# Performance work log

Measured on AMD Instinct MI355X. Metric: run time of the kernel, lower is better.

Reference implementation:

```python
import jax, jax.numpy as jnp
import numpy as np

EMBED = 1024  # point_net_embedding_dim
H1, H2 = 512, 256  # head_hidden_layer_sizes


def _init(key, shape, fan_in):
    return jax.random.normal(key, shape, dtype=jnp.float32) / jnp.sqrt(jnp.float32(fan_in))


def setup_inputs() -> dict:
    key = jax.random.key(0)
    ks = jax.random.split(key, 13)
    B, N = 256, 1024
    x = jax.random.normal(ks[0], (B, N, 3), dtype=jnp.float32)
    # PointNet shared per-point MLP: 3 -> 64 -> 128 -> EMBED (ReLU), max-pool over points
    W1 = _init(ks[1], (3, 64), 3);        b1 = jnp.zeros((64,), jnp.float32)
    W2 = _init(ks[2], (64, 128), 64);     b2 = jnp.zeros((128,), jnp.float32)
    W3 = _init(ks[3], (128, EMBED), 128); b3 = jnp.zeros((EMBED,), jnp.float32)
    # Head MLP: EMBED -> 512 -> 256 -> 9 (no final activation)
    Wh1 = _init(ks[4], (EMBED, H1), EMBED); bh1 = jnp.zeros((H1,), jnp.float32)
    Wh2 = _init(ks[5], (H1, H2), H1);       bh2 = jnp.zeros((H2,), jnp.float32)
    Wh3 = _init(ks[6], (H2, 9), H2);        bh3 = jnp.zeros((9,), jnp.float32)
    return {"x": x, "W1": W1, "b1": b1, "W2": W2, "b2": b2, "W3": W3, "b3": b3,
            "Wh1": Wh1, "bh1": bh1, "Wh2": Wh2, "bh2": bh2, "Wh3": Wh3, "bh3": bh3}


def svd_projection(M):
    # Project raw 3x3 matrices onto SO(3): R = U diag(1,1,det(U V^T)) V^T
    U, S, Vh = jnp.linalg.svd(M, full_matrices=False)
    det = jnp.linalg.det(jnp.einsum('...ij,...jk->...ik', U, Vh))
    d = jnp.stack([jnp.ones_like(det), jnp.ones_like(det), det], axis=-1)  # [..., 3]
    return jnp.einsum('...ij,...j,...jk->...ik', U, d, Vh)


def reference(x, W1, b1, W2, b2, W3, b3, Wh1, bh1, Wh2, bh2, Wh3, bh3):
    # Shared per-point MLP (ReLU), final_activation=ReLU, then max-pool over points
    h = jax.nn.relu(x @ W1 + b1)          # [B, N, 64]
    h = jax.nn.relu(h @ W2 + b2)          # [B, N, 128]
    h = jax.nn.relu(h @ W3 + b3)          # [B, N, EMBED]
    g = jnp.max(h, axis=-2)               # [B, EMBED] global feature
    # Head MLP -> raw 3x3
    z = jax.nn.relu(g @ Wh1 + bh1)
    z = jax.nn.relu(z @ Wh2 + bh2)
    raw = (z @ Wh3 + bh3).reshape(*x.shape[:-2], 3, 3)
    return svd_projection(raw)
```

## Files before the change

kernel.cpp:

```cpp
#include <hip/hip_runtime.h>
#include <math.h>

typedef _Float16 f16;
typedef _Float16 f16x8 __attribute__((ext_vector_type(8)));
typedef float f32x4 __attribute__((ext_vector_type(4)));

__global__ __launch_bounds__(256) void prep_weights(
    const float* __restrict__ W1, const float* __restrict__ b1,
    const float* __restrict__ W2, const float* __restrict__ W3,
    f16* __restrict__ W2t, f16* __restrict__ W3t, float* __restrict__ wpk)
{
    int idx = blockIdx.x * 256 + threadIdx.x;
    int stride = gridDim.x * 256;
    for (int i = idx; i < 1024 * 128; i += stride) {
        int c = i >> 7, k = i & 127;
        W3t[i] = (f16)W3[k * 1024 + c];
    }
    for (int i = idx; i < 128 * 64; i += stride) {
        int c = i >> 6, k = i & 63;
        W2t[i] = (f16)W2[k * 128 + c];
    }
    if (idx < 256) {
        int k = idx >> 2, c = idx & 3;
        wpk[idx] = (c < 3) ? W1[c * 64 + k] : b1[k];
    }
}

__global__ __launch_bounds__(512, 2) void pointnet_fused(
    const float* __restrict__ x,
    const float* __restrict__ wpk,
    const f16* __restrict__ W2t,
    const float* __restrict__ b2,
    const f16* __restrict__ W3t,
    const float* __restrict__ b3,
    float* __restrict__ g)
{
    __shared__ float xs[1024 * 3];
    __shared__ __align__(16) float wls[288];
    __shared__ float b2s[128];
    __shared__ __align__(16) f16 h2s[2][128 * 136];

    int b = blockIdx.x;
    int tid = threadIdx.x;
    int lane = tid & 63, w = tid >> 6;
    int lrow = lane & 15, quad = lane >> 4;
    int wr2 = w & 3, wc2 = w >> 2;

    f16x8 bf3[8][4];
    {
        const f16* base = W3t + (size_t)(w * 128 + lrow) * 128 + quad * 8;
#pragma unroll
        for (int ct = 0; ct < 8; ct++)
#pragma unroll
            for (int kc = 0; kc < 4; kc++)
                bf3[ct][kc] = *(const f16x8*)(base + ct * 16 * 128 + kc * 32);
    }
    f16x8 bf2[4][2];
    {
        const f16* base = W2t + (size_t)(wc2 * 64 + lrow) * 64 + quad * 8;
#pragma unroll
        for (int ct = 0; ct < 4; ct++)
#pragma unroll
            for (int kc2 = 0; kc2 < 2; kc2++)
                bf2[ct][kc2] = *(const f16x8*)(base + ct * 16 * 64 + kc2 * 32);
    }

    {
        const float* xb = x + (size_t)b * 3072;
        for (int i = tid; i < 3072; i += 512) xs[i] = xb[i];
        if (tid < 256) {
            int k = tid >> 2, c = tid & 3;
            wls[(k + (k >> 3)) * 4 + c] = wpk[tid];
        }
        if (tid >= 256 && tid < 384) b2s[tid - 256] = b2[tid - 256];
    }
    __syncthreads();

    const f32x4 z4 = {0.f, 0.f, 0.f, 0.f};
    float cmax[8];
#pragma unroll
    for (int ct = 0; ct < 8; ct++) cmax[ct] = -3.0e38f;

    auto phaseA = [&](int chunk) {
        f16* hb = h2s[chunk & 1];
        int p0 = chunk * 128 + wr2 * 32 + lrow;
        float x00 = xs[p0 * 3], x01 = xs[p0 * 3 + 1], x02 = xs[p0 * 3 + 2];
        int p1 = p0 + 16;
        float x10 = xs[p1 * 3], x11 = xs[p1 * 3 + 1], x12 = xs[p1 * 3 + 2];
        f32x4 acc2[2][4];
#pragma unroll
        for (int kc2 = 0; kc2 < 2; kc2++) {
            f16x8 af2[2];
#pragma unroll
            for (int j = 0; j < 8; j++) {
                int k = kc2 * 32 + quad * 8 + j;
                f32x4 wv = *(const f32x4*)&wls[(k + (k >> 3)) * 4];
                float v0 = fmaf(x02, wv[2], fmaf(x01, wv[1], fmaf(x00, wv[0], wv[3])));
                float v1 = fmaf(x12, wv[2], fmaf(x11, wv[1], fmaf(x10, wv[0], wv[3])));
                af2[0][j] = (f16)fmaxf(v0, 0.f);
                af2[1][j] = (f16)fmaxf(v1, 0.f);
            }
#pragma unroll
            for (int rt = 0; rt < 2; rt++)
#pragma unroll
                for (int ct = 0; ct < 4; ct++)
                    acc2[rt][ct] = __builtin_amdgcn_mfma_f32_16x16x32_f16(
                        af2[rt], bf2[ct][kc2], kc2 ? acc2[rt][ct] : z4, 0, 0, 0);
        }
#pragma unroll
        for (int rt = 0; rt < 2; rt++)
#pragma unroll
            for (int ct = 0; ct < 4; ct++) {
                int col = wc2 * 64 + ct * 16 + lrow;
                float bb = b2s[col];
                int rowb = wr2 * 32 + rt * 16 + quad * 4;
#pragma unroll
                for (int r = 0; r < 4; r++)
                    hb[(rowb + r) * 136 + col] = (f16)fmaxf(acc2[rt][ct][r] + bb, 0.f);
            }
    };

    auto phaseB = [&](int chunk) {
        const f16* hb = h2s[chunk & 1];
#pragma unroll
        for (int rt = 0; rt < 8; rt++) {
            f32x4 acc[8];
#pragma unroll
            for (int kc = 0; kc < 4; kc++) {
                f16x8 af = *(const f16x8*)(hb + (rt * 16 + lrow) * 136 + kc * 32 + quad * 8);
#pragma unroll
                for (int ct = 0; ct < 8; ct++)
                    acc[ct] = __builtin_amdgcn_mfma_f32_16x16x32_f16(
                        af, bf3[ct][kc], kc ? acc[ct] : z4, 0, 0, 0);
            }
#pragma unroll
            for (int ct = 0; ct < 8; ct++) {
                float m01 = fmaxf(acc[ct][0], acc[ct][1]);
                float m23 = fmaxf(acc[ct][2], acc[ct][3]);
                cmax[ct] = fmaxf(cmax[ct], fmaxf(m01, m23));
            }
        }
    };

    phaseA(0);
    __syncthreads();
#pragma unroll 1
    for (int c = 0; c < 7; c++) {
        phaseA(c + 1);
        phaseB(c);
        __syncthreads();
    }
    phaseB(7);

#pragma unroll
    for (int ct = 0; ct < 8; ct++) {
        cmax[ct] = fmaxf(cmax[ct], __shfl_xor(cmax[ct], 16, 64));
        cmax[ct] = fmaxf(cmax[ct], __shfl_xor(cmax[ct], 32, 64));
    }
    if (quad == 0) {
#pragma unroll
        for (int ct = 0; ct < 8; ct++) {
            int cg = w * 128 + ct * 16 + lrow;
            g[(size_t)b * 1024 + cg] = fmaxf(cmax[ct] + b3[cg], 0.f);
        }
    }
}

__global__ __launch_bounds__(256) void head_l1(
    const float* __restrict__ g, const float* __restrict__ Wh1,
    float* __restrict__ zp1)
{
    __shared__ float gs4[4][256];
    int cb = blockIdx.x, bb = blockIdx.y, kc = blockIdx.z;
    int tid = threadIdx.x;
    int b0 = bb * 4;
    int kbase = kc * 256;
#pragma unroll
    for (int j = 0; j < 4; j++) {
        int i = tid + j * 256;
        gs4[i >> 8][i & 255] = g[(size_t)(b0 + (i >> 8)) * 1024 + kbase + (i & 255)];
    }
    __syncthreads();

    int c = cb * 256 + tid;
    float acc[4] = {0.f, 0.f, 0.f, 0.f};
#pragma unroll 1
    for (int k = 0; k < 256; k += 8) {
        float w[8];
#pragma unroll
        for (int j = 0; j < 8; j++) w[j] = Wh1[(size_t)(kbase + k + j) * 512 + c];
#pragma unroll
        for (int r = 0; r < 4; r++) {
            float4 a = *(const float4*)&gs4[r][k];
            float4 bq = *(const float4*)&gs4[r][k + 4];
            acc[r] = fmaf(a.x, w[0], acc[r]);
            acc[r] = fmaf(a.y, w[1], acc[r]);
            acc[r] = fmaf(a.z, w[2], acc[r]);
            acc[r] = fmaf(a.w, w[3], acc[r]);
            acc[r] = fmaf(bq.x, w[4], acc[r]);
            acc[r] = fmaf(bq.y, w[5], acc[r]);
            acc[r] = fmaf(bq.z, w[6], acc[r]);
            acc[r] = fmaf(bq.w, w[7], acc[r]);
        }
    }
#pragma unroll
    for (int r = 0; r < 4; r++)
        zp1[((size_t)kc * 256 + b0 + r) * 512 + c] = acc[r];
}

__global__ __launch_bounds__(256) void head_l2(
    const float* __restrict__ zp1, const float* __restrict__ bh1,
    const float* __restrict__ Wh2, float* __restrict__ zp2)
{
    __shared__ float z1s[2][128];
    int bb = blockIdx.x, kc2 = blockIdx.y;
    int tid = threadIdx.x;
    int b0 = bb * 2;
    int kb = kc2 * 128;
    {
        int row = tid >> 7, kk = tid & 127;
        int col = kb + kk;
        float v = bh1[col];
#pragma unroll
        for (int j = 0; j < 4; j++)
            v += zp1[((size_t)j * 256 + b0 + row) * 512 + col];
        z1s[row][kk] = fmaxf(v, 0.f);
    }
    __syncthreads();

    int c = tid;
    float acc0 = 0.f, acc1 = 0.f;
#pragma unroll 1
    for (int k = 0; k < 128; k += 8) {
        float w[8];
#pragma unroll
        for (int j = 0; j < 8; j++) w[j] = Wh2[(size_t)(kb + k + j) * 256 + c];
        float4 a0 = *(const float4*)&z1s[0][k];
        float4 a1 = *(const float4*)&z1s[0][k + 4];
        float4 d0 = *(const float4*)&z1s[1][k];
        float4 d1 = *(const float4*)&z1s[1][k + 4];
        acc0 = fmaf(a0.x, w[0], acc0);  acc1 = fmaf(d0.x, w[0], acc1);
        acc0 = fmaf(a0.y, w[1], acc0);  acc1 = fmaf(d0.y, w[1], acc1);
        acc0 = fmaf(a0.z, w[2], acc0);  acc1 = fmaf(d0.z, w[2], acc1);
        acc0 = fmaf(a0.w, w[3], acc0);  acc1 = fmaf(d0.w, w[3], acc1);
        acc0 = fmaf(a1.x, w[4], acc0);  acc1 = fmaf(d1.x, w[4], acc1);
        acc0 = fmaf(a1.y, w[5], acc0);  acc1 = fmaf(d1.y, w[5], acc1);
        acc0 = fmaf(a1.z, w[6], acc0);  acc1 = fmaf(d1.z, w[6], acc1);
        acc0 = fmaf(a1.w, w[7], acc0);  acc1 = fmaf(d1.w, w[7], acc1);
    }
    zp2[((size_t)kc2 * 256 + b0    ) * 256 + c] = acc0;
    zp2[((size_t)kc2 * 256 + b0 + 1) * 256 + c] = acc1;
}

__device__ inline void jrot(double S[3][3], double V[3][3], int p, int q)
{
    double apq = S[p][q];
    if (fabs(apq) < 1e-36) return;
    double tau = (S[q][q] - S[p][p]) / (2.0 * apq);
    double t = (tau >= 0.0 ? 1.0 : -1.0) / (fabs(tau) + sqrt(1.0 + tau * tau));
    double c = 1.0 / sqrt(1.0 + t * t);
    double s = t * c;
    for (int k = 0; k < 3; k++) {
        double skp = S[k][p], skq = S[k][q];
        S[k][p] = c * skp - s * skq;  S[k][q] = s * skp + c * skq;
    }
    for (int k = 0; k < 3; k++) {
        double spk = S[p][k], sqk = S[q][k];
        S[p][k] = c * spk - s * sqk;  S[q][k] = s * spk + c * sqk;
    }
    for (int k = 0; k < 3; k++) {
        double vkp = V[k][p], vkq = V[k][q];
        V[k][p] = c * vkp - s * vkq;  V[k][q] = s * vkp + c * vkq;
    }
}

__device__ void svd_so3(const float* Mf, float* Rout)
{
    double M[3][3], S[3][3], V[3][3];
    for (int i = 0; i < 3; i++)
        for (int j = 0; j < 3; j++) M[i][j] = (double)Mf[3 * i + j];
    for (int i = 0; i < 3; i++)
        for (int j = 0; j < 3; j++)
            S[i][j] = M[0][i] * M[0][j] + M[1][i] * M[1][j] + M[2][i] * M[2][j];
    for (int i = 0; i < 3; i++)
        for (int j = 0; j < 3; j++) V[i][j] = (i == j) ? 1.0 : 0.0;
    for (int it = 0; it < 10; it++) {
        jrot(S, V, 0, 1); jrot(S, V, 0, 2); jrot(S, V, 1, 2);
    }
    double lam[3] = {S[0][0], S[1][1], S[2][2]};
    int i0 = 0, i1 = 1, i2 = 2, tt;
    if (lam[i0] < lam[i1]) { tt = i0; i0 = i1; i1 = tt; }
    if (lam[i0] < lam[i2]) { tt = i0; i0 = i2; i2 = tt; }
    if (lam[i1] < lam[i2]) { tt = i1; i1 = i2; i2 = tt; }
    double v0[3], v1[3], v2[3];
    for (int k = 0; k < 3; k++) { v0[k] = V[k][i0]; v1[k] = V[k][i1]; v2[k] = V[k][i2]; }
    double u1[3], u2[3], u3[3];
    for (int i = 0; i < 3; i++) u1[i] = M[i][0] * v0[0] + M[i][1] * v0[1] + M[i][2] * v0[2];
    double n1 = sqrt(u1[0] * u1[0] + u1[1] * u1[1] + u1[2] * u1[2]) + 1e-300;
    for (int i = 0; i < 3; i++) u1[i] /= n1;
    for (int i = 0; i < 3; i++) u2[i] = M[i][0] * v1[0] + M[i][1] * v1[1] + M[i][2] * v1[2];
    double d12 = u1[0] * u2[0] + u1[1] * u2[1] + u1[2] * u2[2];
    for (int i = 0; i < 3; i++) u2[i] -= d12 * u1[i];
    double n2 = sqrt(u2[0] * u2[0] + u2[1] * u2[1] + u2[2] * u2[2]) + 1e-300;
    for (int i = 0; i < 3; i++) u2[i] /= n2;
    u3[0] = u1[1] * u2[2] - u1[2] * u2[1];
    u3[1] = u1[2] * u2[0] - u1[0] * u2[2];
    u3[2] = u1[0] * u2[1] - u1[1] * u2[0];
    double c12x = v1[1] * v2[2] - v1[2] * v2[1];
    double c12y = v1[2] * v2[0] - v1[0] * v2[2];
    double c12z = v1[0] * v2[1] - v1[1] * v2[0];
    double detV = v0[0] * c12x + v0[1] * c12y + v0[2] * c12z;
    for (int i = 0; i < 3; i++)
        for (int j = 0; j < 3; j++)
            Rout[3 * i + j] = (float)(u1[i] * v0[j] + u2[i] * v1[j] + detV * u3[i] * v2[j]);
}

__global__ __launch_bounds__(128) void head_l3_svd(
    const float* __restrict__ zp2, const float* __restrict__ bh2,
    const float* __restrict__ Wh3, const float* __restrict__ bh3,
    float* __restrict__ out)
{
    __shared__ float z2s[8][256];
    __shared__ float wh3s[2304];
    __shared__ float raws[8][12];
    int b0 = blockIdx.x * 8;
    int tid = threadIdx.x;

    for (int i = tid; i < 2304; i += 128) wh3s[i] = Wh3[i];
    for (int i = tid; i < 8 * 256; i += 128) {
        int row = i >> 8, kk = i & 255;
        float v = bh2[kk];
#pragma unroll
        for (int j = 0; j < 4; j++)
            v += zp2[((size_t)j * 256 + b0 + row) * 256 + kk];
        z2s[row][kk] = fmaxf(v, 0.f);
    }
    __syncthreads();

    if (tid < 72) {
        int r = tid / 9, c = tid % 9;
        float acc = bh3[c];
#pragma unroll 8
        for (int k = 0; k < 256; k++) acc = fmaf(z2s[r][k], wh3s[k * 9 + c], acc);
        raws[r][c] = acc;
    }
    __syncthreads();

    if (tid < 8) svd_so3(&raws[tid][0], out + (size_t)(b0 + tid) * 9);
}

extern "C" void kernel_launch(void* const* d_in, const int* in_sizes, int n_in,
                              void* d_out, int out_size, void* d_ws, size_t ws_size,
                              hipStream_t stream)
{
    const float* x   = (const float*)d_in[0];
    const float* W1  = (const float*)d_in[1];
    const float* b1  = (const float*)d_in[2];
    const float* W2  = (const float*)d_in[3];
    const float* b2  = (const float*)d_in[4];
    const float* W3  = (const float*)d_in[5];
    const float* b3  = (const float*)d_in[6];
    const float* Wh1 = (const float*)d_in[7];
    const float* bh1 = (const float*)d_in[8];
    const float* Wh2 = (const float*)d_in[9];
    const float* bh2 = (const float*)d_in[10];
    const float* Wh3 = (const float*)d_in[11];
    const float* bh3 = (const float*)d_in[12];
    float* out = (float*)d_out;

    char* ws = (char*)d_ws;
    f16*   W2t = (f16*)ws;
    f16*   W3t = (f16*)(ws + 65536);
    float* wpk = (float*)(ws + 524288);
    float* g   = (float*)(ws + 1048576);
    float* zp1 = (float*)(ws + 2097152);
    float* zp2 = (float*)(ws + 4194304);

    prep_weights<<<128, 256, 0, stream>>>(W1, b1, W2, W3, W2t, W3t, wpk);
    pointnet_fused<<<256, 512, 0, stream>>>(x, wpk, W2t, b2, W3t, b3, g);
    dim3 gridH1(2, 64, 4);
    head_l1<<<gridH1, 256, 0, stream>>>(g, Wh1, zp1);
    dim3 gridH2(128, 4);
    head_l2<<<gridH2, 256, 0, stream>>>(zp1, bh1, Wh2, zp2);
    head_l3_svd<<<32, 128, 0, stream>>>(zp2, bh2, Wh3, bh3, out);
}
```

Measured before the change: 177.6 us.

## Split point max-pool across two blocks per cloud and fuse head MLP kernels

The per-point MLP kernel now launches two blocks per batch element, each handling 512 points and writing a partial max. The head applies the final max, bias and ReLU, then runs all three head layers and the SVD projection in one kernel. This removes two intermediate launches and the split-K partial buffers, and doubles the block count to fill more CUs. It also raises the launch-bounds occupancy hint and pads the LDS row stride to 140, which adds register pressure and spill risk given the large per-thread W3 fragment array; each head block now streams the full Wh1 and Wh2.

```diff
diff --git a/kernel.cpp b/kernel.cpp
--- a/kernel.cpp
+++ b/kernel.cpp
@@ -4,6 +4,8 @@
 typedef _Float16 f16;
 typedef _Float16 f16x8 __attribute__((ext_vector_type(8)));
 typedef float f32x4 __attribute__((ext_vector_type(4)));
+
+#define H2_STRIDE 140
 
 __global__ __launch_bounds__(256) void prep_weights(
     const float* __restrict__ W1, const float* __restrict__ b1,
@@ -26,21 +28,21 @@
     }
 }
 
-__global__ __launch_bounds__(512, 2) void pointnet_fused(
+__global__ __launch_bounds__(512, 4) void pointnet_fused(
     const float* __restrict__ x,
     const float* __restrict__ wpk,
     const f16* __restrict__ W2t,
     const float* __restrict__ b2,
     const f16* __restrict__ W3t,
-    const float* __restrict__ b3,
-    float* __restrict__ g)
-{
-    __shared__ float xs[1024 * 3];
+    float* __restrict__ gpart)
+{
+    __shared__ float xs[512 * 3];
     __shared__ __align__(16) float wls[288];
     __shared__ float b2s[128];
-    __shared__ __align__(16) f16 h2s[2][128 * 136];
-
-    int b = blockIdx.x;
+    __shared__ __align__(16) f16 h2s[2][128 * H2_STRIDE];
+
+    int bid = blockIdx.x;
+    int b = bid & 255, half = bid >> 8;
     int tid = threadIdx.x;
     int lane = tid & 63, w = tid >> 6;
     int lrow = lane & 15, quad = lane >> 4;
@@ -66,8 +68,8 @@
     }
 
     {
-        const float* xb = x + (size_t)b * 3072;
-        for (int i = tid; i < 3072; i += 512) xs[i] = xb[i];
+        const float* xb = x + (size_t)b * 3072 + (size_t)half * 1536;
+        for (int i = tid; i < 1536; i += 512) xs[i] = xb[i];
         if (tid < 256) {
             int k = tid >> 2, c = tid & 3;
             wls[(k + (k >> 3)) * 4 + c] = wpk[tid];
@@ -116,7 +118,7 @@
                 int rowb = wr2 * 32 + rt * 16 + quad * 4;
 #pragma unroll
                 for (int r = 0; r < 4; r++)
-                    hb[(rowb + r) * 136 + col] = (f16)fmaxf(acc2[rt][ct][r] + bb, 0.f);
+                    hb[(rowb + r) * H2_STRIDE + col] = (f16)fmaxf(acc2[rt][ct][r] + bb, 0.f);
             }
     };
 
@@ -127,7 +129,7 @@
             f32x4 acc[8];
 #pragma unroll
             for (int kc = 0; kc < 4; kc++) {
-                f16x8 af = *(const f16x8*)(hb + (rt * 16 + lrow) * 136 + kc * 32 + quad * 8);
+                f16x8 af = *(const f16x8*)(hb + (rt * 16 + lrow) * H2_STRIDE + kc * 32 + quad * 8);
 #pragma unroll
                 for (int ct = 0; ct < 8; ct++)
                     acc[ct] = __builtin_amdgcn_mfma_f32_16x16x32_f16(
@@ -145,12 +147,12 @@
     phaseA(0);
     __syncthreads();
 #pragma unroll 1
-    for (int c = 0; c < 7; c++) {
+    for (int c = 0; c < 3; c++) {
         phaseA(c + 1);
         phaseB(c);
         __syncthreads();
     }
-    phaseB(7);
+    phaseB(3);
 
 #pragma unroll
     for (int ct = 0; ct < 8; ct++) {
@@ -161,95 +163,91 @@
 #pragma unroll
         for (int ct = 0; ct < 8; ct++) {
             int cg = w * 128 + ct * 16 + lrow;
-            g[(size_t)b * 1024 + cg] = fmaxf(cmax[ct] + b3[cg], 0.f);
-        }
-    }
-}
-
-__global__ __launch_bounds__(256) void head_l1(
-    const float* __restrict__ g, const float* __restrict__ Wh1,
-    float* __restrict__ zp1)
-{
-    __shared__ float gs4[4][256];
-    int cb = blockIdx.x, bb = blockIdx.y, kc = blockIdx.z;
+            gpart[((size_t)(half * 256 + b)) * 1024 + cg] = cmax[ct];
+        }
+    }
+}
+
+__global__ __launch_bounds__(512) void head_fused(
+    const float* __restrict__ gpart,
+    const float* __restrict__ b3,
+    const float* __restrict__ Wh1, const float* __restrict__ bh1,
+    const float* __restrict__ Wh2, const float* __restrict__ bh2,
+    const float* __restrict__ Wh3, const float* __restrict__ bh3,
+    float* __restrict__ out)
+{
+    __shared__ float gs[2][1024];
+    __shared__ float z1[2][512];
+    __shared__ float z2[2][256];
+    __shared__ float raws[2][12];
+
+    int b0 = blockIdx.x * 2;
     int tid = threadIdx.x;
-    int b0 = bb * 4;
-    int kbase = kc * 256;
-#pragma unroll
-    for (int j = 0; j < 4; j++) {
-        int i = tid + j * 256;
-        gs4[i >> 8][i & 255] = g[(size_t)(b0 + (i >> 8)) * 1024 + kbase + (i & 255)];
-    }
-    __syncthreads();
-
-    int c = cb * 256 + tid;
-    float acc[4] = {0.f, 0.f, 0.f, 0.f};
-#pragma unroll 1
-    for (int k = 0; k < 256; k += 8) {
-        float w[8];
-#pragma unroll
-        for (int j = 0; j < 8; j++) w[j] = Wh1[(size_t)(kbase + k + j) * 512 + c];
-#pragma unroll
-        for (int r = 0; r < 4; r++) {
-            float4 a = *(const float4*)&gs4[r][k];
-            float4 bq = *(const float4*)&gs4[r][k + 4];
-            acc[r] = fmaf(a.x, w[0], acc[r]);
-            acc[r] = fmaf(a.y, w[1], acc[r]);
-            acc[r] = fmaf(a.z, w[2], acc[r]);
-            acc[r] = fmaf(a.w, w[3], acc[r]);
-            acc[r] = fmaf(bq.x, w[4], acc[r]);
-            acc[r] = fmaf(bq.y, w[5], acc[r]);
-            acc[r] = fmaf(bq.z, w[6], acc[r]);
-            acc[r] = fmaf(bq.w, w[7], acc[r]);
-        }
-    }
-#pragma unroll
-    for (int r = 0; r < 4; r++)
-        zp1[((size_t)kc * 256 + b0 + r) * 512 + c] = acc[r];
-}
-
-__global__ __launch_bounds__(256) void head_l2(
-    const float* __restrict__ zp1, const float* __restrict__ bh1,
-    const float* __restrict__ Wh2, float* __restrict__ zp2)
-{
-    __shared__ float z1s[2][128];
-    int bb = blockIdx.x, kc2 = blockIdx.y;
-    int tid = threadIdx.x;
-    int b0 = bb * 2;
-    int kb = kc2 * 128;
-    {
-        int row = tid >> 7, kk = tid & 127;
-        int col = kb + kk;
-        float v = bh1[col];
-#pragma unroll
-        for (int j = 0; j < 4; j++)
-            v += zp1[((size_t)j * 256 + b0 + row) * 512 + col];
-        z1s[row][kk] = fmaxf(v, 0.f);
-    }
-    __syncthreads();
-
-    int c = tid;
-    float acc0 = 0.f, acc1 = 0.f;
-#pragma unroll 1
-    for (int k = 0; k < 128; k += 8) {
-        float w[8];
-#pragma unroll
-        for (int j = 0; j < 8; j++) w[j] = Wh2[(size_t)(kb + k + j) * 256 + c];
-        float4 a0 = *(const float4*)&z1s[0][k];
-        float4 a1 = *(const float4*)&z1s[0][k + 4];
-        float4 d0 = *(const float4*)&z1s[1][k];
-        float4 d1 = *(const float4*)&z1s[1][k + 4];
-        acc0 = fmaf(a0.x, w[0], acc0);  acc1 = fmaf(d0.x, w[0], acc1);
-        acc0 = fmaf(a0.y, w[1], acc0);  acc1 = fmaf(d0.y, w[1], acc1);
-        acc0 = fmaf(a0.z, w[2], acc0);  acc1 = fmaf(d0.z, w[2], acc1);
-        acc0 = fmaf(a0.w, w[3], acc0);  acc1 = fmaf(d0.w, w[3], acc1);
-        acc0 = fmaf(a1.x, w[4], acc0);  acc1 = fmaf(d1.x, w[4], acc1);
-        acc0 = fmaf(a1.y, w[5], acc0);  acc1 = fmaf(d1.y, w[5], acc1);
-        acc0 = fmaf(a1.z, w[6], acc0);  acc1 = fmaf(d1.z, w[6], acc1);
-        acc0 = fmaf(a1.w, w[7], acc0);  acc1 = fmaf(d1.w, w[7], acc1);
-    }
-    zp2[((size_t)kc2 * 256 + b0    ) * 256 + c] = acc0;
-    zp2[((size_t)kc2 * 256 + b0 + 1) * 256 + c] = acc1;
+
+    for (int i = tid; i < 2048; i += 512) {
+        int r = i >> 10, col = i & 1023;
+        int bb = b0 + r;
+        float p0 = gpart[(size_t)bb * 1024 + col];
+        float p1 = gpart[(size_t)(256 + bb) * 1024 + col];
+        gs[r][col] = fmaxf(fmaxf(p0, p1) + b3[col], 0.f);
+    }
+    __syncthreads();
+
+    {
+        float a0 = bh1[tid], a1 = a0;
+        const float* wp = Wh1 + tid;
+#pragma unroll 2
+        for (int k = 0; k < 1024; k += 4) {
+            float4 g0 = *(const float4*)&gs[0][k];
+            float4 g1 = *(const float4*)&gs[1][k];
+            float w0 = wp[(size_t)(k    ) * 512];
+            float w1 = wp[(size_t)(k + 1) * 512];
+            float w2 = wp[(size_t)(k + 2) * 512];
+            float w3 = wp[(size_t)(k + 3) * 512];
+            a0 = fmaf(g0.x, w0, a0);  a1 = fmaf(g1.x, w0, a1);
+            a0 = fmaf(g0.y, w1, a0);  a1 = fmaf(g1.y, w1, a1);
+            a0 = fmaf(g0.z, w2, a0);  a1 = fmaf(g1.z, w2, a1);
+            a0 = fmaf(g0.w, w3, a0);  a1 = fmaf(g1.w, w3, a1);
+        }
+        z1[0][tid] = fmaxf(a0, 0.f);
+        z1[1][tid] = fmaxf(a1, 0.f);
+    }
+    __syncthreads();
+
+    {
+        int r = tid >> 8, c = tid & 255;
+        float acc = bh2[c];
+        const float* wp = Wh2 + c;
+#pragma unroll 2
+        for (int k = 0; k < 512; k += 4) {
+            float4 zv = *(const float4*)&z1[r][k];
+            float w0 = wp[(size_t)(k    ) * 256];
+            float w1 = wp[(size_t)(k + 1) * 256];
+            float w2 = wp[(size_t)(k + 2) * 256];
+            float w3 = wp[(size_t)(k + 3) * 256];
+            acc = fmaf(zv.x, w0, acc);
+            acc = fmaf(zv.y, w1, acc);
+            acc = fmaf(zv.z, w2, acc);
+            acc = fmaf(zv.w, w3, acc);
+        }
+        z2[r][c] = fmaxf(acc, 0.f);
+    }
+    __syncthreads();
+
+    if (tid < 18) {
+        int r = tid / 9, c = tid - r * 9;
+        float acc = bh3[c];
+#pragma unroll 8
+        for (int k = 0; k < 256; k++)
+            acc = fmaf(z2[r][k], Wh3[k * 9 + c], acc);
+        raws[r][c] = acc;
+    }
+    __syncthreads();
+
+    if (tid < 2) {
+        extern __device__ void svd_so3(const float*, float*);
+        svd_so3(&raws[tid][0], out + (size_t)(b0 + tid) * 9);
+    }
 }
 
 __device__ inline void jrot(double S[3][3], double V[3][3], int p, int q)
@@ -315,40 +313,6 @@
             Rout[3 * i + j] = (float)(u1[i] * v0[j] + u2[i] * v1[j] + detV * u3[i] * v2[j]);
 }
 
-__global__ __launch_bounds__(128) void head_l3_svd(
-    const float* __restrict__ zp2, const float* __restrict__ bh2,
-    const float* __restrict__ Wh3, const float* __restrict__ bh3,
-    float* __restrict__ out)
-{
-    __shared__ float z2s[8][256];
-    __shared__ float wh3s[2304];
-    __shared__ float raws[8][12];
-    int b0 = blockIdx.x * 8;
-    int tid = threadIdx.x;
-
-    for (int i = tid; i < 2304; i += 128) wh3s[i] = Wh3[i];
-    for (int i = tid; i < 8 * 256; i += 128) {
-        int row = i >> 8, kk = i & 255;
-        float v = bh2[kk];
-#pragma unroll
-        for (int j = 0; j < 4; j++)
-            v += zp2[((size_t)j * 256 + b0 + row) * 256 + kk];
-        z2s[row][kk] = fmaxf(v, 0.f);
-    }
-    __syncthreads();
-
-    if (tid < 72) {
-        int r = tid / 9, c = tid % 9;
-        float acc = bh3[c];
-#pragma unroll 8
-        for (int k = 0; k < 256; k++) acc = fmaf(z2s[r][k], wh3s[k * 9 + c], acc);
-        raws[r][c] = acc;
-    }
-    __syncthreads();
-
-    if (tid < 8) svd_so3(&raws[tid][0], out + (size_t)(b0 + tid) * 9);
-}
-
 extern "C" void kernel_launch(void* const* d_in, const int* in_sizes, int n_in,
                               void* d_out, int out_size, void* d_ws, size_t ws_size,
                               hipStream_t stream)
@@ -369,18 +333,12 @@
     float* out = (float*)d_out;
 
     char* ws = (char*)d_ws;
-    f16*   W2t = (f16*)ws;
-    f16*   W3t = (f16*)(ws + 65536);
-    float* wpk = (float*)(ws + 524288);
-    float* g   = (float*)(ws + 1048576);
-    float* zp1 = (float*)(ws + 2097152);
-    float* zp2 = (float*)(ws + 4194304);
+    f16*   W2t   = (f16*)ws;
+    f16*   W3t   = (f16*)(ws + 65536);
+    float* wpk   = (float*)(ws + 524288);
+    float* gpart = (float*)(ws + 1048576);
 
     prep_weights<<<128, 256, 0, stream>>>(W1, b1, W2, W3, W2t, W3t, wpk);
-    pointnet_fused<<<256, 512, 0, stream>>>(x, wpk, W2t, b2, W3t, b3, g);
-    dim3 gridH1(2, 64, 4);
-    head_l1<<<gridH1, 256, 0, stream>>>(g, Wh1, zp1);
-    dim3 gridH2(128, 4);
-    head_l2<<<gridH2, 256, 0, stream>>>(zp1, bh1, Wh2, zp2);
-    head_l3_svd<<<32, 128, 0, stream>>>(zp2, bh2, Wh3, bh3, out);
-}
+    pointnet_fused<<<512, 512, 0, stream>>>(x, wpk, W2t, b2, W3t, gpart);
+    head_fused<<<128, 512, 0, stream>>>(gpart, b3, Wh1, bh1, Wh2, bh2, Wh3, bh3, out);
+}
```

Measured after the change: 612.0 us. 245% more time.
